# Kernel optimization log

Measured on AMD Instinct MI355X. Metric: run time of the kernel, lower is better.

The kernel has to match this reference:

```python
import jax, jax.numpy as jnp
import numpy as np

BASE_WEIGHT = 0.01
ADAPTATION_RATE = 0.1
EPS = 1e-8
N = 16384
H = 64


def setup_inputs() -> dict:
    key = jax.random.key(0)
    k1, k2, k3, k4 = jax.random.split(key, 4)
    return {
        "x_input": jax.random.normal(k1, (N,), dtype=jnp.float32),
        "targets": jax.random.normal(k2, (N,), dtype=jnp.float32),
        "w1": jax.random.normal(k3, (H,), dtype=jnp.float32) * 0.5,
        "b1": jnp.zeros((H,), dtype=jnp.float32),
        "w2": jax.random.normal(k4, (H,), dtype=jnp.float32) * 0.5,
        "b2": jnp.zeros((1,), dtype=jnp.float32),
    }


def _mlp(x, w1, b1, w2, b2):
    # elementwise 1 -> H -> 1 tanh MLP: predictions y_i = f(x_i)
    h = jnp.tanh(x[:, None] * w1 + b1)  # [N, H]
    return h @ w2 + b2[0]               # [N]


def _local_density(x):
    # NxN pairwise abs-diff matrix, top-3 smallest per row
    diff = jnp.abs(x[:, None] - x[None, :]) + EPS       # [N, N]
    neg_knn, _ = jax.lax.top_k(-diff, 3)                # smallest 3 via negation
    knn = -neg_knn                                       # [N, 3]
    dens = 1.0 / (knn.mean(axis=1, keepdims=True) + EPS)  # [N, 1]
    return dens / (dens.max() + EPS)


def reference(x_input, targets, w1, b1, w2, b2):
    f_sum = lambda xx: jnp.sum(_mlp(xx, w1, b1, w2, b2))
    predictions = _mlp(x_input, w1, b1, w2, b2)
    mse_loss = jnp.mean((predictions - targets) ** 2)

    # torch.autograd.grad(..., grad_outputs=ones) twice == grad of summed output twice
    dy_dx_sum = lambda xx: jnp.sum(jax.grad(f_sum)(xx))
    d2y_dx2 = jax.grad(dy_dx_sum)(x_input)               # [N]

    density = _local_density(x_input)                    # [N, 1]
    adaptive_weights = 1.0 + ADAPTATION_RATE * density   # [N, 1]
    # torch broadcasts [N,1]*[N] -> [N,N]; mean of that outer product equals
    # mean(weights) * mean(d2**2) exactly, so compute it without the NxN alloc.
    curvature_penalty = BASE_WEIGHT * (jnp.mean(adaptive_weights) * jnp.mean(d2y_dx2 ** 2))

    total_loss = mse_loss + curvature_penalty
    return (total_loss, mse_loss, curvature_penalty)
```

## Files before the change

kernel.cpp:

```cpp
#include <hip/hip_runtime.h>
#include <math.h>

#define NPTS 16384
#define HDIM 64
#define NSEG 8
#define SEGLEN (NPTS / NSEG)
#define IBLK 512
#define NBLK (NPTS / 64)
#define EPSF 1e-8f
#define FMAX3 3.402823466e38f

__device__ __forceinline__ void ins2(float& m1, float& m2, float d) {
    m2 = __builtin_amdgcn_fmed3f(d, m1, m2);
    m1 = fminf(d, m1);
}

__global__ __launch_bounds__(IBLK) void fused_kernel(
    const float* __restrict__ x, const float* __restrict__ tg,
    const float* __restrict__ w1, const float* __restrict__ b1,
    const float* __restrict__ w2, const float* __restrict__ b2,
    float* __restrict__ acc, float* __restrict__ out) {
    __shared__ float sA[NSEG][64], sB[NSEG][64];
    const int t = threadIdx.x;
    const int lane = t & 63;
    const int w = t >> 6;
    const int ib = blockIdx.x;
    const int i = ib * 64 + lane;
    const float xi = x[i];
    const float* __restrict__ xc = x + w * SEGLEN;

    float m1 = FMAX3, m2 = FMAX3;
    if (w == (ib >> 5)) {
        float m3 = FMAX3;
#pragma unroll 16
        for (int k = 0; k < SEGLEN; ++k) {
            float d = fabsf(xi - xc[k]);
            m3 = __builtin_amdgcn_fmed3f(d, m2, m3);
            m2 = __builtin_amdgcn_fmed3f(d, m1, m2);
            m1 = fminf(d, m1);
        }
        m1 = m2;
        m2 = m3;
    } else {
#pragma unroll 16
        for (int k = 0; k < SEGLEN; ++k) {
            float d = fabsf(xi - xc[k]);
            ins2(m1, m2, d);
        }
    }
    sA[w][lane] = m1;
    sB[w][lane] = m2;
    __syncthreads();

    if (t < 64) {
        float M1 = FMAX3, M2 = FMAX3;
#pragma unroll
        for (int s = 0; s < NSEG; ++s) {
            ins2(M1, M2, sA[s][t]);
            ins2(M1, M2, sB[s][t]);
        }
        float dens = 1.0f / ((M1 + M2) * (1.0f / 3.0f) + 2.0f * EPSF);

        float y = b2[0];
        float d2a = 0.0f;
#pragma unroll 8
        for (int j = 0; j < HDIM; ++j) {
            float a1 = w1[j], bb = b1[j], a2 = w2[j];
            float u = fmaf(xi, a1, bb);
            float e = __expf(2.0f * u);
            float r = __builtin_amdgcn_rcpf(e + 1.0f);
            float tt = fmaf(-2.0f, r, 1.0f);
            y = fmaf(a2, tt, y);
            float g = 2.0f * tt * fmaf(tt, tt, -1.0f);
            d2a = fmaf(a2 * a1 * a1, g, d2a);
        }
        float diff = y - tg[i];
        float rs_mse = diff * diff;
        float rs_d2 = d2a * d2a;
        float rs_dn = dens, rmx = dens;
        for (int o = 32; o > 0; o >>= 1) {
            rs_mse += __shfl_down(rs_mse, o);
            rs_d2 += __shfl_down(rs_d2, o);
            rs_dn += __shfl_down(rs_dn, o);
            rmx = fmaxf(rmx, __shfl_down(rmx, o));
        }
        if (t == 0) {
            atomicAdd(&acc[0], rs_mse);
            atomicAdd(&acc[1], rs_d2);
            atomicAdd(&acc[2], rs_dn);
            atomicMax((unsigned int*)&acc[3], __float_as_uint(rmx));
            __threadfence();
            unsigned int ticket = atomicAdd((unsigned int*)&acc[4], 1u);
            if (ticket == NBLK - 1) {
                float s_mse = atomicAdd(&acc[0], 0.0f);
                float s_d2 = atomicAdd(&acc[1], 0.0f);
                float s_dn = atomicAdd(&acc[2], 0.0f);
                float dmax = __uint_as_float(atomicMax((unsigned int*)&acc[3], 0u));
                float mse = s_mse * (1.0f / NPTS);
                float md2 = s_d2 * (1.0f / NPTS);
                float mean_density = (s_dn * (1.0f / NPTS)) / (dmax + EPSF);
                float penalty = 0.01f * (1.0f + 0.1f * mean_density) * md2;
                out[0] = mse + penalty;
                out[1] = mse;
                out[2] = penalty;
            }
        }
    }
}

extern "C" void kernel_launch(void* const* d_in, const int* in_sizes, int n_in,
                              void* d_out, int out_size, void* d_ws, size_t ws_size,
                              hipStream_t stream) {
    const float* x = (const float*)d_in[0];
    const float* tg = (const float*)d_in[1];
    const float* w1 = (const float*)d_in[2];
    const float* b1 = (const float*)d_in[3];
    const float* w2 = (const float*)d_in[4];
    const float* b2 = (const float*)d_in[5];
    float* out = (float*)d_out;
    float* acc = (float*)d_ws;

    hipMemsetAsync(acc, 0, 8 * sizeof(float), stream);
    hipLaunchKernelGGL(fused_kernel, dim3(NBLK), dim3(IBLK), 0, stream,
                       x, tg, w1, b1, w2, b2, acc, out);
}
```

Baseline: 120.6 us.

## Split kNN scan into many chunked blocks and a separate merge kernel

Replaces the single fused kernel with two kernels. The first runs many blocks, each scanning one chunk of 512 candidate points for 256 query points, and writes per-chunk top-2 partial results to workspace. The second merges the 32 partials per point, then runs the MLP and the reductions. This is meant to raise occupancy and fill the GPU better than 256 large blocks did, at the cost of writing and re-reading about 4 MB of partials and an extra kernel launch.

```diff
diff --git a/kernel.cpp b/kernel.cpp
--- a/kernel.cpp
+++ b/kernel.cpp
@@ -3,10 +3,10 @@
 
 #define NPTS 16384
 #define HDIM 64
-#define NSEG 8
-#define SEGLEN (NPTS / NSEG)
-#define IBLK 512
-#define NBLK (NPTS / 64)
+#define JCH 32
+#define CHUNK (NPTS / JCH)
+#define IBLK 256
+#define NIB (NPTS / IBLK)
 #define EPSF 1e-8f
 #define FMAX3 3.402823466e38f
 
@@ -15,25 +15,19 @@
     m1 = fminf(d, m1);
 }
 
-__global__ __launch_bounds__(IBLK) void fused_kernel(
-    const float* __restrict__ x, const float* __restrict__ tg,
-    const float* __restrict__ w1, const float* __restrict__ b1,
-    const float* __restrict__ w2, const float* __restrict__ b2,
-    float* __restrict__ acc, float* __restrict__ out) {
-    __shared__ float sA[NSEG][64], sB[NSEG][64];
-    const int t = threadIdx.x;
-    const int lane = t & 63;
-    const int w = t >> 6;
-    const int ib = blockIdx.x;
-    const int i = ib * 64 + lane;
+__global__ __launch_bounds__(IBLK) void knn2_kernel(
+    const float* __restrict__ x, float2* __restrict__ part) {
+    const int jc = blockIdx.x & (JCH - 1);
+    const int ic = blockIdx.x >> 5;
+    const int i = ic * IBLK + threadIdx.x;
     const float xi = x[i];
-    const float* __restrict__ xc = x + w * SEGLEN;
+    const float* __restrict__ xc = x + jc * CHUNK;
 
     float m1 = FMAX3, m2 = FMAX3;
-    if (w == (ib >> 5)) {
+    if (jc == (ic >> 1)) {
         float m3 = FMAX3;
 #pragma unroll 16
-        for (int k = 0; k < SEGLEN; ++k) {
+        for (int k = 0; k < CHUNK; ++k) {
             float d = fabsf(xi - xc[k]);
             m3 = __builtin_amdgcn_fmed3f(d, m2, m3);
             m2 = __builtin_amdgcn_fmed3f(d, m1, m2);
@@ -43,67 +37,75 @@
         m2 = m3;
     } else {
 #pragma unroll 16
-        for (int k = 0; k < SEGLEN; ++k) {
+        for (int k = 0; k < CHUNK; ++k) {
             float d = fabsf(xi - xc[k]);
             ins2(m1, m2, d);
         }
     }
-    sA[w][lane] = m1;
-    sB[w][lane] = m2;
-    __syncthreads();
+    part[jc * NPTS + i] = make_float2(m1, m2);
+}
 
-    if (t < 64) {
-        float M1 = FMAX3, M2 = FMAX3;
+__global__ __launch_bounds__(64) void merge_kernel(
+    const float* __restrict__ x, const float* __restrict__ tg,
+    const float* __restrict__ w1, const float* __restrict__ b1,
+    const float* __restrict__ w2, const float* __restrict__ b2,
+    const float2* __restrict__ part, float* __restrict__ acc,
+    float* __restrict__ out) {
+    const int t = threadIdx.x;
+    const int i = blockIdx.x * 64 + t;
+
+    float m1 = FMAX3, m2 = FMAX3;
 #pragma unroll
-        for (int s = 0; s < NSEG; ++s) {
-            ins2(M1, M2, sA[s][t]);
-            ins2(M1, M2, sB[s][t]);
-        }
-        float dens = 1.0f / ((M1 + M2) * (1.0f / 3.0f) + 2.0f * EPSF);
+    for (int jc = 0; jc < JCH; ++jc) {
+        float2 p = part[jc * NPTS + i];
+        ins2(m1, m2, p.x);
+        ins2(m1, m2, p.y);
+    }
+    float dens = 1.0f / ((m1 + m2) * (1.0f / 3.0f) + 2.0f * EPSF);
 
-        float y = b2[0];
-        float d2a = 0.0f;
+    const float xi = x[i];
+    float y = b2[0];
+    float d2a = 0.0f;
 #pragma unroll 8
-        for (int j = 0; j < HDIM; ++j) {
-            float a1 = w1[j], bb = b1[j], a2 = w2[j];
-            float u = fmaf(xi, a1, bb);
-            float e = __expf(2.0f * u);
-            float r = __builtin_amdgcn_rcpf(e + 1.0f);
-            float tt = fmaf(-2.0f, r, 1.0f);
-            y = fmaf(a2, tt, y);
-            float g = 2.0f * tt * fmaf(tt, tt, -1.0f);
-            d2a = fmaf(a2 * a1 * a1, g, d2a);
-        }
-        float diff = y - tg[i];
-        float rs_mse = diff * diff;
-        float rs_d2 = d2a * d2a;
-        float rs_dn = dens, rmx = dens;
-        for (int o = 32; o > 0; o >>= 1) {
-            rs_mse += __shfl_down(rs_mse, o);
-            rs_d2 += __shfl_down(rs_d2, o);
-            rs_dn += __shfl_down(rs_dn, o);
-            rmx = fmaxf(rmx, __shfl_down(rmx, o));
-        }
-        if (t == 0) {
-            atomicAdd(&acc[0], rs_mse);
-            atomicAdd(&acc[1], rs_d2);
-            atomicAdd(&acc[2], rs_dn);
-            atomicMax((unsigned int*)&acc[3], __float_as_uint(rmx));
-            __threadfence();
-            unsigned int ticket = atomicAdd((unsigned int*)&acc[4], 1u);
-            if (ticket == NBLK - 1) {
-                float s_mse = atomicAdd(&acc[0], 0.0f);
-                float s_d2 = atomicAdd(&acc[1], 0.0f);
-                float s_dn = atomicAdd(&acc[2], 0.0f);
-                float dmax = __uint_as_float(atomicMax((unsigned int*)&acc[3], 0u));
-                float mse = s_mse * (1.0f / NPTS);
-                float md2 = s_d2 * (1.0f / NPTS);
-                float mean_density = (s_dn * (1.0f / NPTS)) / (dmax + EPSF);
-                float penalty = 0.01f * (1.0f + 0.1f * mean_density) * md2;
-                out[0] = mse + penalty;
-                out[1] = mse;
-                out[2] = penalty;
-            }
+    for (int j = 0; j < HDIM; ++j) {
+        float a1 = w1[j], bb = b1[j], a2 = w2[j];
+        float u = fmaf(xi, a1, bb);
+        float e = __expf(2.0f * u);
+        float r = __builtin_amdgcn_rcpf(e + 1.0f);
+        float tt = fmaf(-2.0f, r, 1.0f);
+        y = fmaf(a2, tt, y);
+        float g = 2.0f * tt * fmaf(tt, tt, -1.0f);
+        d2a = fmaf(a2 * a1 * a1, g, d2a);
+    }
+    float diff = y - tg[i];
+    float rs_mse = diff * diff;
+    float rs_d2 = d2a * d2a;
+    float rs_dn = dens, rmx = dens;
+    for (int o = 32; o > 0; o >>= 1) {
+        rs_mse += __shfl_down(rs_mse, o);
+        rs_d2 += __shfl_down(rs_d2, o);
+        rs_dn += __shfl_down(rs_dn, o);
+        rmx = fmaxf(rmx, __shfl_down(rmx, o));
+    }
+    if (t == 0) {
+        atomicAdd(&acc[0], rs_mse);
+        atomicAdd(&acc[1], rs_d2);
+        atomicAdd(&acc[2], rs_dn);
+        atomicMax((unsigned int*)&acc[3], __float_as_uint(rmx));
+        __threadfence();
+        unsigned int ticket = atomicAdd((unsigned int*)&acc[4], 1u);
+        if (ticket == (NPTS / 64) - 1) {
+            float s_mse = atomicAdd(&acc[0], 0.0f);
+            float s_d2 = atomicAdd(&acc[1], 0.0f);
+            float s_dn = atomicAdd(&acc[2], 0.0f);
+            float dmax = __uint_as_float(atomicMax((unsigned int*)&acc[3], 0u));
+            float mse = s_mse * (1.0f / NPTS);
+            float md2 = s_d2 * (1.0f / NPTS);
+            float mean_density = (s_dn * (1.0f / NPTS)) / (dmax + EPSF);
+            float penalty = 0.01f * (1.0f + 0.1f * mean_density) * md2;
+            out[0] = mse + penalty;
+            out[1] = mse;
+            out[2] = penalty;
         }
     }
 }
@@ -118,9 +120,12 @@
     const float* w2 = (const float*)d_in[4];
     const float* b2 = (const float*)d_in[5];
     float* out = (float*)d_out;
-    float* acc = (float*)d_ws;
+    float* wsf = (float*)d_ws;
+    float2* part = (float2*)wsf;
+    float* acc = wsf + 2 * JCH * NPTS;
 
     hipMemsetAsync(acc, 0, 8 * sizeof(float), stream);
-    hipLaunchKernelGGL(fused_kernel, dim3(NBLK), dim3(IBLK), 0, stream,
-                       x, tg, w1, b1, w2, b2, acc, out);
+    hipLaunchKernelGGL(knn2_kernel, dim3(NIB * JCH), dim3(IBLK), 0, stream, x, part);
+    hipLaunchKernelGGL(merge_kernel, dim3(NPTS / 64), dim3(64), 0, stream,
+                       x, tg, w1, b1, w2, b2, part, acc, out);
 }
```

Result: faster. 106.5 us (-11.6%).
